# Kernel optimization log

Measured on AMD Instinct MI355X. Metric: run time of the kernel, lower is better.

The kernel has to match this reference:

```python
import jax, jax.numpy as jnp
import numpy as np

DIM, NH, WS, SHIFT = 192, 6, 7, 3
HD = DIM // NH


def setup_inputs() -> dict:
    key = jax.random.key(0)
    ks = jax.random.split(key, 5)
    x = jax.random.normal(ks[0], (8, DIM, 224, 224), dtype=jnp.float32)
    s = 1.0 / np.sqrt(DIM)
    qkv_w = jax.random.normal(ks[1], (3 * DIM, DIM), dtype=jnp.float32) * s
    qkv_b = jnp.zeros((3 * DIM,), dtype=jnp.float32)
    proj_w = jax.random.normal(ks[2], (DIM, DIM), dtype=jnp.float32) * s
    proj_b = jnp.zeros((DIM,), dtype=jnp.float32)
    return {"x": x, "qkv_w": qkv_w, "qkv_b": qkv_b, "proj_w": proj_w, "proj_b": proj_b}


def reference(x, qkv_w, qkv_b, proj_w, proj_b):
    B, C, H, W = x.shape
    ws, nh, hd, shift = WS, NH, HD, SHIFT
    pad_h = (ws - H % ws) % ws
    pad_w = (ws - W % ws) % ws
    if pad_h or pad_w:
        x = jnp.pad(x, ((0, 0), (0, 0), (0, pad_h), (0, pad_w)))
    Hp, Wp = H + pad_h, W + pad_w
    if shift > 0:
        x = jnp.roll(x, (-shift, -shift), axis=(2, 3))
    # window partition: [B,C,Hp,Wp] -> [B*nWh*nWw, ws*ws, C]
    xw = (x.reshape(B, C, Hp // ws, ws, Wp // ws, ws)
           .transpose(0, 2, 4, 3, 5, 1)
           .reshape(-1, ws * ws, C))
    qkv = xw @ qkv_w.T + qkv_b                      # [N, 49, 3C]
    qkv = qkv.reshape(-1, ws * ws, 3, nh, hd).transpose(2, 0, 3, 1, 4)
    q, k, v = qkv[0], qkv[1], qkv[2]                # [N, nh, 49, hd]
    scale = hd ** (-0.5)
    attn = jnp.einsum('nhqd,nhkd->nhqk', q, k) * scale
    attn = jax.nn.softmax(attn, axis=-1)
    out = jnp.einsum('nhqk,nhkd->nhqd', attn, v)    # [N, nh, 49, hd]
    out = out.transpose(0, 2, 1, 3).reshape(-1, ws * ws, C)
    out = out @ proj_w.T + proj_b
    # window merge: [N, ws*ws, C] -> [B, C, Hp, Wp]
    out = (out.reshape(B, Hp // ws, Wp // ws, ws, ws, C)
              .transpose(0, 5, 1, 3, 2, 4)
              .reshape(B, C, Hp, Wp))
    if shift > 0:
        out = jnp.roll(out, (shift, shift), axis=(2, 3))
    return out[:, :, :H, :W]
```

## Files before the change

### kernel.cpp

```cpp
#include <hip/hip_runtime.h>
#include <hip/hip_fp16.h>

#define DIM   192
#define NH    6
#define WSZ   7
#define SHIFT 3
#define TOK   49
#define HW    224
#define NWIN  8192

typedef _Float16 half_t;
typedef _Float16 half8 __attribute__((ext_vector_type(8)));
typedef float    f32x4 __attribute__((ext_vector_type(4)));

#define WQKV_HALFS  (6*3*96*64)
#define WPROJ_HALFS (6*192*32)

__global__ __launch_bounds__(256) void prep_weights(const float* __restrict__ qkv_w,
                                                    const float* __restrict__ proj_w,
                                                    half_t* __restrict__ wp) {
  int e = blockIdx.x * 256 + threadIdx.x;
  if (e < WQKV_HALFS) {
    int h  = e / (3*96*64);
    int r1 = e % (3*96*64);
    int kc = r1 / (96*64);
    int r2 = r1 % (96*64);
    int r  = r2 / 64;
    int kl = r2 % 64;
    int g  = (r < 32) ? (h*32 + r) : (r < 64 ? (192 + h*32 + (r-32)) : (384 + h*32 + (r-64)));
    float v = qkv_w[g*192 + kc*64 + kl];
    int cs = (kl >> 3) ^ (r & 7);
    wp[((h*3 + kc)*96 + r)*64 + cs*8 + (kl & 7)] = (half_t)v;
  } else {
    int e2 = e - WQKV_HALFS;
    if (e2 < WPROJ_HALFS) {
      int h  = e2 / (192*32);
      int r  = (e2 >> 5) % 192;
      int kl = e2 & 31;
      wp[WQKV_HALFS + e2] = (half_t)proj_w[r*192 + h*32 + kl];
    }
  }
}

#define OFF_X   0
#define OFF_Q   19600
#define OFF_K   23760
#define OFF_VT  27920
#define OFF_AOH 32016
#define OFF_W   36176
#define SMEM_BYTES 48464

__global__ __launch_bounds__(512, 4) void swin_attn(const float* __restrict__ x,
                                                    const float* __restrict__ qkv_b,
                                                    const float* __restrict__ proj_b,
                                                    const half_t* __restrict__ wp,
                                                    float* __restrict__ out) {
  __shared__ __align__(16) unsigned char smem[SMEM_BYTES];
  half_t* s_x   = (half_t*)(smem + OFF_X);
  half_t* s_q   = (half_t*)(smem + OFF_Q);
  half_t* s_k   = (half_t*)(smem + OFF_K);
  half_t* s_vt  = (half_t*)(smem + OFF_VT);
  half_t* s_aoh = (half_t*)(smem + OFF_AOH);
  half_t* s_w   = (half_t*)(smem + OFF_W);
  half_t* s_p   = (half_t*)(smem + OFF_W);
  float*  s_out = (float*)(smem);

  int bid = blockIdx.x;
  bid = (bid & 7) * 1024 + (bid >> 3);
  int b  = bid >> 10;
  int wh = (bid >> 5) & 31;
  int ww = bid & 31;

  int tid  = threadIdx.x;
  int wave = tid >> 6;
  int lane = tid & 63;
  int lg   = lane >> 4;
  int lr   = lane & 15;
  int m    = wave & 3;
  int nh   = wave >> 2;
  int mrow0 = m * 16;

  const float* xb = x + (size_t)b * DIM * HW * HW;

  for (int e = tid; e < TOK*DIM; e += 512) {
    int c = e / TOK;
    int r = e - c*TOK;
    int i = r / WSZ, j = r - i*WSZ;
    int hh = wh*WSZ + i + SHIFT; if (hh >= HW) hh -= HW;
    int wp2 = ww*WSZ + j + SHIFT; if (wp2 >= HW) wp2 -= HW;
    s_x[r*200 + c] = (half_t)xb[(size_t)c*HW*HW + hh*HW + wp2];
  }

  f32x4 pacc[6];
  #pragma unroll
  for (int n = 0; n < 6; ++n) { pacc[n][0]=0.f; pacc[n][1]=0.f; pacc[n][2]=0.f; pacc[n][3]=0.f; }

  const float qscale = 0.17677669529663687f;
  const half_t* wproj = wp + WQKV_HALFS;
  const half8 ZERO8 = {0,0,0,0,0,0,0,0};
  const uint4* wsrc = (const uint4*)wp;

  uint4 r0 = wsrc[tid], r1;
  if (tid < 256) r1 = wsrc[512 + tid];

  for (int h = 0; h < NH; ++h) {
    f32x4 acc[3];
    #pragma unroll
    for (int n = 0; n < 3; ++n) { acc[n][0]=0.f; acc[n][1]=0.f; acc[n][2]=0.f; acc[n][3]=0.f; }
    for (int kc = 0; kc < 3; ++kc) {
      int cidx = h*3 + kc;
      __syncthreads();
      {
        uint4* dst = (uint4*)s_w;
        dst[tid] = r0;
        if (tid < 256) dst[512 + tid] = r1;
        if (cidx < 17) {
          const uint4* nx = wsrc + (size_t)(cidx + 1) * 768;
          r0 = nx[tid];
          if (tid < 256) r1 = nx[512 + tid];
        }
      }
      __syncthreads();
      #pragma unroll
      for (int ks = 0; ks < 2; ++ks) {
        int row = mrow0 + lr;
        int rowc = row > 48 ? 48 : row;
        half8 a = *(const half8*)(s_x + rowc*200 + kc*64 + ks*32 + lg*8);
        if (row > 48) a = ZERO8;
        #pragma unroll
        for (int i = 0; i < 3; ++i) {
          int rr = (nh*3 + i)*16 + lr;
          half8 bf = *(const half8*)(s_w + rr*64 + (((ks*4 + lg) ^ (rr & 7)) * 8));
          acc[i] = __builtin_amdgcn_mfma_f32_16x16x32_f16(a, bf, acc[i], 0, 0, 0);
        }
      }
    }
    #pragma unroll
    for (int i = 0; i < 3; ++i) {
      int nt   = nh*3 + i;
      int sect = nt >> 1;
      int chl  = (nt & 1)*16 + lr;
      float bia = qkv_b[sect*192 + h*32 + chl];
      if (sect == 0) {
        #pragma unroll
        for (int jj = 0; jj < 4; ++jj) {
          int tok = mrow0 + lg*4 + jj;
          if (tok < 52) s_q[tok*40 + chl] = (half_t)((acc[i][jj] + bia) * qscale);
        }
      } else if (sect == 1) {
        #pragma unroll
        for (int jj = 0; jj < 4; ++jj) {
          int tok = mrow0 + lg*4 + jj;
          if (tok < 52) s_k[tok*40 + chl] = (half_t)(acc[i][jj] + bia);
        }
      } else {
        int tok0 = mrow0 + lg*4;
        union { half_t h4[4]; uint2 u; } pk2;
        #pragma unroll
        for (int jj = 0; jj < 4; ++jj) {
          int tok = tok0 + jj;
          float v = (tok < TOK) ? (acc[i][jj] + bia) : 0.f;
          pk2.h4[jj] = (half_t)v;
        }
        int chunk = (tok0 >> 3) ^ (chl & 7);
        *(uint2*)(s_vt + chl*64 + chunk*8 + (tok0 & 7)) = pk2.u;
      }
    }
    __syncthreads();

    f32x4 sacc[4];
    #pragma unroll
    for (int n = 0; n < 4; ++n) { sacc[n][0]=0.f; sacc[n][1]=0.f; sacc[n][2]=0.f; sacc[n][3]=0.f; }
    {
      half8 a = *(const half8*)(s_q + (mrow0 + lr)*40 + lg*8);
      #pragma unroll
      for (int n = 0; n < 4; ++n) {
        half8 bf = *(const half8*)(s_k + (n*16 + lr)*40 + lg*8);
        sacc[n] = __builtin_amdgcn_mfma_f32_16x16x32_f16(a, bf, sacc[n], 0, 0, 0);
      }
    }
    if (lr >= 1) {
      #pragma unroll
      for (int jj = 0; jj < 4; ++jj) sacc[3][jj] = -1e30f;
    }
    float rl[4];
    #pragma unroll
    for (int jj = 0; jj < 4; ++jj) {
      float mx = fmaxf(fmaxf(sacc[0][jj], sacc[1][jj]), fmaxf(sacc[2][jj], sacc[3][jj]));
      #pragma unroll
      for (int d = 1; d < 16; d <<= 1) mx = fmaxf(mx, __shfl_xor(mx, d));
      float p[4], ssum = 0.f;
      #pragma unroll
      for (int n = 0; n < 4; ++n) { p[n] = __expf(sacc[n][jj] - mx); ssum += p[n]; }
      #pragma unroll
      for (int d = 1; d < 16; d <<= 1) ssum += __shfl_xor(ssum, d);
      rl[jj] = 1.f / ssum;
      if (nh == 0) {
        int tok = mrow0 + lg*4 + jj;
        if (tok < 52) {
          #pragma unroll
          for (int n = 0; n < 4; ++n)
            s_p[tok*72 + n*16 + lr] = (half_t)p[n];
        }
      }
    }
    __syncthreads();

    f32x4 oacc;
    oacc[0]=0.f; oacc[1]=0.f; oacc[2]=0.f; oacc[3]=0.f;
    #pragma unroll
    for (int ks = 0; ks < 2; ++ks) {
      half8 a = *(const half8*)(s_p + (mrow0 + lr)*72 + ks*32 + lg*8);
      int d = nh*16 + lr;
      int chunk = (ks*4 + lg) ^ (d & 7);
      half8 bf = *(const half8*)(s_vt + d*64 + chunk*8);
      oacc = __builtin_amdgcn_mfma_f32_16x16x32_f16(a, bf, oacc, 0, 0, 0);
    }
    #pragma unroll
    for (int jj = 0; jj < 4; ++jj) {
      int tok = mrow0 + lg*4 + jj;
      if (tok < 52) s_aoh[tok*40 + nh*16 + lr] = (half_t)(oacc[jj] * rl[jj]);
    }
    __syncthreads();

    {
      half8 a = *(const half8*)(s_aoh + (mrow0 + lr)*40 + lg*8);
      #pragma unroll
      for (int i2 = 0; i2 < 6; ++i2) {
        int ch = (nh*6 + i2)*16 + lr;
        half8 bf = *(const half8*)(wproj + ((size_t)h*192 + ch)*32 + lg*8);
        pacc[i2] = __builtin_amdgcn_mfma_f32_16x16x32_f16(a, bf, pacc[i2], 0, 0, 0);
      }
    }
  }
  __syncthreads();

  #pragma unroll
  for (int i2 = 0; i2 < 6; ++i2) {
    int ch = (nh*6 + i2)*16 + lr;
    float bia = proj_b[ch];
    #pragma unroll
    for (int jj = 0; jj < 4; ++jj) {
      int tok = mrow0 + lg*4 + jj;
      if (tok < TOK) s_out[ch*52 + tok] = pacc[i2][jj] + bia;
    }
  }
  __syncthreads();
  float* ob = out + (size_t)b * DIM * HW * HW;
  for (int e = tid; e < TOK*DIM; e += 512) {
    int c = e / TOK;
    int r = e - c*TOK;
    int i = r / WSZ, j = r - i*WSZ;
    int hh = wh*WSZ + i + SHIFT; if (hh >= HW) hh -= HW;
    int wp2 = ww*WSZ + j + SHIFT; if (wp2 >= HW) wp2 -= HW;
    ob[(size_t)c*HW*HW + hh*HW + wp2] = s_out[c*52 + r];
  }
}

extern "C" void kernel_launch(void* const* d_in, const int* in_sizes, int n_in,
                              void* d_out, int out_size, void* d_ws, size_t ws_size,
                              hipStream_t stream) {
  const float* x      = (const float*)d_in[0];
  const float* qkv_w  = (const float*)d_in[1];
  const float* qkv_b  = (const float*)d_in[2];
  const float* proj_w = (const float*)d_in[3];
  const float* proj_b = (const float*)d_in[4];
  half_t* wpk = (half_t*)d_ws;

  prep_weights<<<576, 256, 0, stream>>>(qkv_w, proj_w, wpk);
  swin_attn<<<NWIN, 512, 0, stream>>>(x, qkv_b, proj_b, wpk, (float*)d_out);
}
```

Baseline: 739.8 us.

## Keep X fragments in registers, read QKV weights from global, shrink LDS

```diff
diff --git a/kernel.cpp b/kernel.cpp
--- a/kernel.cpp
+++ b/kernel.cpp
@@ -1,19 +1,19 @@
 #include <hip/hip_runtime.h>
 #include <hip/hip_fp16.h>
 
-#define DIM   192
-#define NH    6
-#define WSZ   7
-#define SHIFT 3
-#define TOK   49
-#define HW    224
-#define NWIN  8192
+#define DIM     192
+#define NHEADS  6
+#define WSZ     7
+#define SHIFT   3
+#define TOK     49
+#define HW      224
+#define NWIN    8192
 
 typedef _Float16 half_t;
 typedef _Float16 half8 __attribute__((ext_vector_type(8)));
 typedef float    f32x4 __attribute__((ext_vector_type(4)));
 
-#define WQKV_HALFS  (6*3*96*64)
+#define WQKV_HALFS  (6*96*192)
 #define WPROJ_HALFS (6*192*32)
 
 __global__ __launch_bounds__(256) void prep_weights(const float* __restrict__ qkv_w,
@@ -21,49 +21,39 @@
                                                     half_t* __restrict__ wp) {
   int e = blockIdx.x * 256 + threadIdx.x;
   if (e < WQKV_HALFS) {
-    int h  = e / (3*96*64);
-    int r1 = e % (3*96*64);
-    int kc = r1 / (96*64);
-    int r2 = r1 % (96*64);
-    int r  = r2 / 64;
-    int kl = r2 % 64;
-    int g  = (r < 32) ? (h*32 + r) : (r < 64 ? (192 + h*32 + (r-32)) : (384 + h*32 + (r-64)));
-    float v = qkv_w[g*192 + kc*64 + kl];
-    int cs = (kl >> 3) ^ (r & 7);
-    wp[((h*3 + kc)*96 + r)*64 + cs*8 + (kl & 7)] = (half_t)v;
+    int h  = e / 18432;
+    int r1 = e % 18432;
+    int r  = r1 / 192;
+    int kk = r1 % 192;
+    int sect = r >> 5;
+    int chl  = r & 31;
+    wp[e] = (half_t)qkv_w[(sect*192 + h*32 + chl)*192 + kk];
   } else {
     int e2 = e - WQKV_HALFS;
     if (e2 < WPROJ_HALFS) {
-      int h  = e2 / (192*32);
-      int r  = (e2 >> 5) % 192;
+      int h  = e2 / 6144;
+      int rr = (e2 >> 5) % 192;
       int kl = e2 & 31;
-      wp[WQKV_HALFS + e2] = (half_t)proj_w[r*192 + h*32 + kl];
+      wp[WQKV_HALFS + e2] = (half_t)proj_w[rr*192 + h*32 + kl];
     }
   }
 }
 
-#define OFF_X   0
-#define OFF_Q   19600
-#define OFF_K   23760
-#define OFF_VT  27920
-#define OFF_AOH 32016
-#define OFF_W   36176
-#define SMEM_BYTES 48464
-
-__global__ __launch_bounds__(512, 4) void swin_attn(const float* __restrict__ x,
+#define SMEM_BYTES 39936
+
+__global__ __launch_bounds__(512, 6) void swin_attn(const float* __restrict__ x,
                                                     const float* __restrict__ qkv_b,
                                                     const float* __restrict__ proj_b,
                                                     const half_t* __restrict__ wp,
                                                     float* __restrict__ out) {
   __shared__ __align__(16) unsigned char smem[SMEM_BYTES];
-  half_t* s_x   = (half_t*)(smem + OFF_X);
-  half_t* s_q   = (half_t*)(smem + OFF_Q);
-  half_t* s_k   = (half_t*)(smem + OFF_K);
-  half_t* s_vt  = (half_t*)(smem + OFF_VT);
-  half_t* s_aoh = (half_t*)(smem + OFF_AOH);
-  half_t* s_w   = (half_t*)(smem + OFF_W);
-  half_t* s_p   = (half_t*)(smem + OFF_W);
-  float*  s_out = (float*)(smem);
+  half_t* s_x   = (half_t*)smem;
+  half_t* s_q   = (half_t*)smem;
+  half_t* s_k   = (half_t*)(smem + 4160);
+  half_t* s_vt  = (half_t*)(smem + 8320);
+  half_t* s_aoh = (half_t*)(smem + 12416);
+  half_t* s_p   = (half_t*)(smem + 16576);
+  float*  s_out = (float*)smem;
 
   int bid = blockIdx.x;
   bid = (bid & 7) * 1024 + (bid >> 3);
@@ -77,19 +67,43 @@
   int lg   = lane >> 4;
   int lr   = lane & 15;
   int m    = wave & 3;
-  int nh   = wave >> 2;
-  int mrow0 = m * 16;
+  int nhf  = wave >> 2;
+  int mrow0 = m << 4;
 
   const float* xb = x + (size_t)b * DIM * HW * HW;
 
-  for (int e = tid; e < TOK*DIM; e += 512) {
-    int c = e / TOK;
-    int r = e - c*TOK;
-    int i = r / WSZ, j = r - i*WSZ;
-    int hh = wh*WSZ + i + SHIFT; if (hh >= HW) hh -= HW;
-    int wp2 = ww*WSZ + j + SHIFT; if (wp2 >= HW) wp2 -= HW;
-    s_x[r*200 + c] = (half_t)xb[(size_t)c*HW*HW + hh*HW + wp2];
-  }
+  {
+    int c = tid / 49;
+    int r = tid - c * 49;
+    for (int it = 0; it < 19; ++it) {
+      if (c < 192) {
+        int i = r / 7, j = r - i * 7;
+        int hh = wh*WSZ + i + SHIFT; if (hh >= HW) hh -= HW;
+        int w2 = ww*WSZ + j + SHIFT; if (w2 >= HW) w2 -= HW;
+        s_x[r*200 + c] = (half_t)xb[(size_t)c*(HW*HW) + hh*HW + w2];
+      }
+      r += 22; c += 10;
+      if (r >= 49) { r -= 49; ++c; }
+    }
+  }
+  __syncthreads();
+
+  const half8 HZ = {0,0,0,0,0,0,0,0};
+  half8 afr[6];
+  {
+    int arow = mrow0 + lr;
+    const half_t* ax = s_x + (arow > 48 ? 48 : arow)*200 + lg*8;
+    #pragma unroll
+    for (int kc = 0; kc < 3; ++kc)
+      #pragma unroll
+      for (int ks = 0; ks < 2; ++ks)
+        afr[kc*2 + ks] = *(const half8*)(ax + kc*64 + ks*32);
+    if (arow > 48) {
+      #pragma unroll
+      for (int u = 0; u < 6; ++u) afr[u] = HZ;
+    }
+  }
+  __syncthreads();
 
   f32x4 pacc[6];
   #pragma unroll
@@ -97,47 +111,31 @@
 
   const float qscale = 0.17677669529663687f;
   const half_t* wproj = wp + WQKV_HALFS;
-  const half8 ZERO8 = {0,0,0,0,0,0,0,0};
-  const uint4* wsrc = (const uint4*)wp;
-
-  uint4 r0 = wsrc[tid], r1;
-  if (tid < 256) r1 = wsrc[512 + tid];
-
-  for (int h = 0; h < NH; ++h) {
+
+  for (int h = 0; h < NHEADS; ++h) {
     f32x4 acc[3];
     #pragma unroll
     for (int n = 0; n < 3; ++n) { acc[n][0]=0.f; acc[n][1]=0.f; acc[n][2]=0.f; acc[n][3]=0.f; }
-    for (int kc = 0; kc < 3; ++kc) {
-      int cidx = h*3 + kc;
-      __syncthreads();
-      {
-        uint4* dst = (uint4*)s_w;
-        dst[tid] = r0;
-        if (tid < 256) dst[512 + tid] = r1;
-        if (cidx < 17) {
-          const uint4* nx = wsrc + (size_t)(cidx + 1) * 768;
-          r0 = nx[tid];
-          if (tid < 256) r1 = nx[512 + tid];
-        }
-      }
-      __syncthreads();
-      #pragma unroll
-      for (int ks = 0; ks < 2; ++ks) {
-        int row = mrow0 + lr;
-        int rowc = row > 48 ? 48 : row;
-        half8 a = *(const half8*)(s_x + rowc*200 + kc*64 + ks*32 + lg*8);
-        if (row > 48) a = ZERO8;
-        #pragma unroll
-        for (int i = 0; i < 3; ++i) {
-          int rr = (nh*3 + i)*16 + lr;
-          half8 bf = *(const half8*)(s_w + rr*64 + (((ks*4 + lg) ^ (rr & 7)) * 8));
-          acc[i] = __builtin_amdgcn_mfma_f32_16x16x32_f16(a, bf, acc[i], 0, 0, 0);
-        }
+    {
+      const half_t* wqh = wp + (size_t)h*18432 + ((nhf*3)*16 + lr)*192 + lg*8;
+      #pragma unroll
+      for (int kc = 0; kc < 3; ++kc) {
+        half8 bfr[6];
+        #pragma unroll
+        for (int i = 0; i < 3; ++i)
+          #pragma unroll
+          for (int ks = 0; ks < 2; ++ks)
+            bfr[i*2+ks] = *(const half8*)(wqh + i*3072 + kc*64 + ks*32);
+        #pragma unroll
+        for (int ks = 0; ks < 2; ++ks)
+          #pragma unroll
+          for (int i = 0; i < 3; ++i)
+            acc[i] = __builtin_amdgcn_mfma_f32_16x16x32_f16(afr[kc*2+ks], bfr[i*2+ks], acc[i], 0, 0, 0);
       }
     }
     #pragma unroll
     for (int i = 0; i < 3; ++i) {
-      int nt   = nh*3 + i;
+      int nt   = nhf*3 + i;
       int sect = nt >> 1;
       int chl  = (nt & 1)*16 + lr;
       float bia = qkv_b[sect*192 + h*32 + chl];
@@ -168,39 +166,36 @@
     }
     __syncthreads();
 
-    f32x4 sacc[4];
-    #pragma unroll
-    for (int n = 0; n < 4; ++n) { sacc[n][0]=0.f; sacc[n][1]=0.f; sacc[n][2]=0.f; sacc[n][3]=0.f; }
-    {
-      half8 a = *(const half8*)(s_q + (mrow0 + lr)*40 + lg*8);
+    if (nhf == 0) {
+      f32x4 sacc[4];
+      #pragma unroll
+      for (int n = 0; n < 4; ++n) { sacc[n][0]=0.f; sacc[n][1]=0.f; sacc[n][2]=0.f; sacc[n][3]=0.f; }
+      half8 aq = *(const half8*)(s_q + (mrow0 + lr)*40 + lg*8);
       #pragma unroll
       for (int n = 0; n < 4; ++n) {
         half8 bf = *(const half8*)(s_k + (n*16 + lr)*40 + lg*8);
-        sacc[n] = __builtin_amdgcn_mfma_f32_16x16x32_f16(a, bf, sacc[n], 0, 0, 0);
-      }
-    }
-    if (lr >= 1) {
-      #pragma unroll
-      for (int jj = 0; jj < 4; ++jj) sacc[3][jj] = -1e30f;
-    }
-    float rl[4];
-    #pragma unroll
-    for (int jj = 0; jj < 4; ++jj) {
-      float mx = fmaxf(fmaxf(sacc[0][jj], sacc[1][jj]), fmaxf(sacc[2][jj], sacc[3][jj]));
-      #pragma unroll
-      for (int d = 1; d < 16; d <<= 1) mx = fmaxf(mx, __shfl_xor(mx, d));
-      float p[4], ssum = 0.f;
-      #pragma unroll
-      for (int n = 0; n < 4; ++n) { p[n] = __expf(sacc[n][jj] - mx); ssum += p[n]; }
-      #pragma unroll
-      for (int d = 1; d < 16; d <<= 1) ssum += __shfl_xor(ssum, d);
-      rl[jj] = 1.f / ssum;
-      if (nh == 0) {
+        sacc[n] = __builtin_amdgcn_mfma_f32_16x16x32_f16(aq, bf, sacc[n], 0, 0, 0);
+      }
+      if (lr >= 1) {
+        #pragma unroll
+        for (int jj = 0; jj < 4; ++jj) sacc[3][jj] = -1e30f;
+      }
+      #pragma unroll
+      for (int jj = 0; jj < 4; ++jj) {
+        float mx = fmaxf(fmaxf(sacc[0][jj], sacc[1][jj]), fmaxf(sacc[2][jj], sacc[3][jj]));
+        #pragma unroll
+        for (int d = 1; d < 16; d <<= 1) mx = fmaxf(mx, __shfl_xor(mx, d));
+        float p[4], ssum = 0.f;
+        #pragma unroll
+        for (int n = 0; n < 4; ++n) { p[n] = __expf(sacc[n][jj] - mx); ssum += p[n]; }
+        #pragma unroll
+        for (int d = 1; d < 16; d <<= 1) ssum += __shfl_xor(ssum, d);
+        float rl = 1.f / ssum;
         int tok = mrow0 + lg*4 + jj;
         if (tok < 52) {
           #pragma unroll
           for (int n = 0; n < 4; ++n)
-            s_p[tok*72 + n*16 + lr] = (half_t)p[n];
+            s_p[tok*72 + n*16 + lr] = (half_t)(p[n] * rl);
         }
       }
     }
@@ -211,7 +206,7 @@
     #pragma unroll
     for (int ks = 0; ks < 2; ++ks) {
       half8 a = *(const half8*)(s_p + (mrow0 + lr)*72 + ks*32 + lg*8);
-      int d = nh*16 + lr;
+      int d = nhf*16 + lr;
       int chunk = (ks*4 + lg) ^ (d & 7);
       half8 bf = *(const half8*)(s_vt + d*64 + chunk*8);
       oacc = __builtin_amdgcn_mfma_f32_16x16x32_f16(a, bf, oacc, 0, 0, 0);
@@ -219,16 +214,16 @@
     #pragma unroll
     for (int jj = 0; jj < 4; ++jj) {
       int tok = mrow0 + lg*4 + jj;
-      if (tok < 52) s_aoh[tok*40 + nh*16 + lr] = (half_t)(oacc[jj] * rl[jj]);
+      if (tok < 52) s_aoh[tok*40 + nhf*16 + lr] = (half_t)oacc[jj];
     }
     __syncthreads();
 
     {
       half8 a = *(const half8*)(s_aoh + (mrow0 + lr)*40 + lg*8);
+      const half_t* wph = wproj + ((size_t)h*192 + (nhf*6)*16 + lr)*32 + lg*8;
       #pragma unroll
       for (int i2 = 0; i2 < 6; ++i2) {
-        int ch = (nh*6 + i2)*16 + lr;
-        half8 bf = *(const half8*)(wproj + ((size_t)h*192 + ch)*32 + lg*8);
+        half8 bf = *(const half8*)(wph + i2*512);
         pacc[i2] = __builtin_amdgcn_mfma_f32_16x16x32_f16(a, bf, pacc[i2], 0, 0, 0);
       }
     }
@@ -237,7 +232,7 @@
 
   #pragma unroll
   for (int i2 = 0; i2 < 6; ++i2) {
-    int ch = (nh*6 + i2)*16 + lr;
+    int ch = (nhf*6 + i2)*16 + lr;
     float bia = proj_b[ch];
     #pragma unroll
     for (int jj = 0; jj < 4; ++jj) {
@@ -246,14 +241,21 @@
     }
   }
   __syncthreads();
+
   float* ob = out + (size_t)b * DIM * HW * HW;
-  for (int e = tid; e < TOK*DIM; e += 512) {
-    int c = e / TOK;
-    int r = e - c*TOK;
-    int i = r / WSZ, j = r - i*WSZ;
-    int hh = wh*WSZ + i + SHIFT; if (hh >= HW) hh -= HW;
-    int wp2 = ww*WSZ + j + SHIFT; if (wp2 >= HW) wp2 -= HW;
-    ob[(size_t)c*HW*HW + hh*HW + wp2] = s_out[c*52 + r];
+  {
+    int c = tid / 49;
+    int r = tid - c * 49;
+    for (int it = 0; it < 19; ++it) {
+      if (c < 192) {
+        int i = r / 7, j = r - i * 7;
+        int hh = wh*WSZ + i + SHIFT; if (hh >= HW) hh -= HW;
+        int w2 = ww*WSZ + j + SHIFT; if (w2 >= HW) w2 -= HW;
+        ob[(size_t)c*(HW*HW) + hh*HW + w2] = s_out[c*52 + r];
+      }
+      r += 22; c += 10;
+      if (r >= 49) { r -= 49; ++c; }
+    }
   }
 }
 
```

Result: slower. 2.080 ms (+181.1%).
